# Performance work log

Measured on AMD Instinct MI355X. Metric: run time of the kernel, lower is better.

## Reference

```python
import jax, jax.numpy as jnp
import numpy as np

N = 100000
E = 1600000
IN_F = 128
HIDDEN = 128
HEADS = 2
N_CLASSES = 40
NEG_SLOPE = 0.2
BN_EPS = 1e-5


def setup_inputs() -> dict:
    key = jax.random.key(0)
    ks = jax.random.split(key, 12)
    c1 = HIDDEN // HEADS  # 64
    c2 = N_CLASSES        # 40 per head, concat=False
    inp = {
        "x": jax.random.normal(ks[0], (N, IN_F), dtype=jnp.float32),
        "edge_index": jax.random.randint(ks[1], (2, E), 0, N, dtype=jnp.int32),
        # layer 1 GATConv params
        "W1": jax.random.normal(ks[2], (IN_F, HEADS * c1), dtype=jnp.float32) * 0.05,
        "att_src1": jax.random.normal(ks[3], (HEADS, c1), dtype=jnp.float32) * 0.05,
        "att_dst1": jax.random.normal(ks[4], (HEADS, c1), dtype=jnp.float32) * 0.05,
        "b1": jnp.zeros((HEADS * c1,), dtype=jnp.float32),
        # BatchNorm params
        "gamma": jnp.ones((HIDDEN,), dtype=jnp.float32),
        "beta": jnp.zeros((HIDDEN,), dtype=jnp.float32),
        # layer 2 GATConv params (concat=False)
        "W2": jax.random.normal(ks[5], (HIDDEN, HEADS * c2), dtype=jnp.float32) * 0.05,
        "att_src2": jax.random.normal(ks[6], (HEADS, c2), dtype=jnp.float32) * 0.05,
        "att_dst2": jax.random.normal(ks[7], (HEADS, c2), dtype=jnp.float32) * 0.05,
        "b2": jnp.zeros((c2,), dtype=jnp.float32),
    }
    return inp


def gat_conv(x, src, dst, W, att_src, att_dst, bias, heads, concat):
    n = x.shape[0]
    h = (x @ W).reshape(n, heads, -1)             # [N, H, C]
    a_src = jnp.sum(h * att_src[None], axis=-1)   # [N, H]
    a_dst = jnp.sum(h * att_dst[None], axis=-1)   # [N, H]
    alpha = jax.nn.leaky_relu(a_src[src] + a_dst[dst], NEG_SLOPE)  # [E, H]
    # numerically-stable segment softmax over edges grouped by dst
    amax = jax.ops.segment_max(alpha, dst, num_segments=n)
    e = jnp.exp(alpha - amax[dst])
    denom = jax.ops.segment_sum(e, dst, num_segments=n)
    w = e / denom[dst]                            # [E, H]
    msg = h[src] * w[:, :, None]                  # [E, H, C]
    out = jax.ops.segment_sum(msg, dst, num_segments=n)  # [N, H, C]
    if concat:
        out = out.reshape(n, -1)
    else:
        out = out.mean(axis=1)
    return out + bias


def batch_norm(x, gamma, beta):
    mean = x.mean(axis=0)
    var = x.var(axis=0)
    return (x - mean) * jax.lax.rsqrt(var + BN_EPS) * gamma + beta


def reference(x, edge_index, W1, att_src1, att_dst1, b1, gamma, beta,
              W2, att_src2, att_dst2, b2):
    n = x.shape[0]
    # PyG GATConv default: add self-loops
    loops = jnp.arange(n, dtype=edge_index.dtype)
    src = jnp.concatenate([edge_index[0], loops])
    dst = jnp.concatenate([edge_index[1], loops])
    h = gat_conv(x, src, dst, W1, att_src1, att_dst1, b1, HEADS, concat=True)
    h = batch_norm(h, gamma, beta)
    h = gat_conv(h, src, dst, W2, att_src2, att_dst2, b2, HEADS, concat=False)
    return jax.nn.log_softmax(h, axis=1)
```

## Files before the change

kernel.cpp:

```cpp
#include <hip/hip_runtime.h>
#include <hip/hip_bf16.h>
#include <hip/hip_fp16.h>
#include <stdint.h>

#define N_NODES 100000
#define N_EDGES 1600000
#define ET (N_EDGES + N_NODES)
#define HID 128
#define C2 40
#define F2 80
#define NEG 0.2f
#define BN_EPS 1e-5f
#define NBUCK 391
#define BCAP 6144
#define NBB 640
#define EPB ((ET + NBB - 1) / NBB)
#define CHK 512

typedef __hip_bfloat16 bf16;
typedef __attribute__((ext_vector_type(8))) short s8v;
typedef __attribute__((ext_vector_type(4))) float f4v;
typedef __attribute__((ext_vector_type(4))) unsigned int u4v;
typedef __attribute__((ext_vector_type(2))) unsigned int u2v;

__device__ __forceinline__ float b2f(bf16 v){ return __bfloat162float(v); }
__device__ __forceinline__ float rdf(const void* p, size_t i, int isb){
    return isb ? b2f(((const bf16*)p)[i]) : ((const float*)p)[i];
}
__device__ __forceinline__ unsigned short f2bb(float v){
    bf16 h = __float2bfloat16(v);
    return *(unsigned short*)&h;
}
__device__ __forceinline__ uint32_t pack2(float a, float b){
    return (uint32_t)f2bb(a) | ((uint32_t)f2bb(b) << 16);
}
__device__ __forceinline__ uint32_t packh2(float a, float b){
    return (uint32_t)__half_as_ushort(__float2half(a))
         | ((uint32_t)__half_as_ushort(__float2half(b)) << 16);
}
__device__ __forceinline__ float lo16(uint32_t u){ return __uint_as_float(u << 16); }
__device__ __forceinline__ float hi16(uint32_t u){ return __uint_as_float(u & 0xFFFF0000u); }
__device__ __forceinline__ float hcvt(uint32_t w, int sh){
    return __half2float(__ushort_as_half((unsigned short)((w >> sh) & 0xFFFFu)));
}

__global__ __launch_bounds__(256) void k_init(
    const uint32_t* __restrict__ w1bits, int* __restrict__ flag,
    int* __restrict__ gcur, float* __restrict__ stats)
{
    __shared__ int cnt;
    int t = threadIdx.x;
    if (t == 0) cnt = 0;
    __syncthreads();
    uint32_t b = w1bits[t];
    float lo = __uint_as_float((b & 0xFFFFu) << 16);
    float a = fabsf(lo);
    if (a > 1e-8f && a < 1.0f) atomicAdd(&cnt, 1);
    for (int i = t; i < NBUCK; i += 256) gcur[i] = 0;
    stats[t] = 0.f;
    __syncthreads();
    if (t == 0) *flag = (cnt >= 192) ? 1 : 0;
}

__global__ __launch_bounds__(256) void k_gemm1(
    const void* __restrict__ x, const void* __restrict__ W1,
    const void* __restrict__ attS, const void* __restrict__ attD,
    const int* __restrict__ flag, unsigned short* __restrict__ h1,
    float* __restrict__ aS, float* __restrict__ aD)
{
    __shared__ __attribute__((aligned(16))) unsigned short wT[128*132];
    const int isb = *flag;
    const int tid = threadIdx.x;
    if (isb) {
        const unsigned short* w = (const unsigned short*)W1;
        for (int idx = tid; idx < 128*128; idx += 256){
            int k = idx >> 7, n = idx & 127;
            wT[n*132 + k] = w[idx];
        }
    } else {
        const float* w = (const float*)W1;
        for (int idx = tid; idx < 128*128; idx += 256){
            int k = idx >> 7, n = idx & 127;
            wT[n*132 + k] = f2bb(w[idx]);
        }
    }
    __syncthreads();

    const int w4 = tid >> 6, lane = tid & 63, quad = lane >> 4, l16 = lane & 15;
    const int rowbase = blockIdx.x*32 + (w4 >> 1)*16;
    const int colbase = (w4 & 1)*64;
    const int head = w4 & 1;

    s8v bfr[4][4];
    float asv[4], adv[4];
    #pragma unroll
    for (int ct = 0; ct < 4; ct++){
        int n = colbase + ct*16 + l16;
        asv[ct] = rdf(attS, n, isb);
        adv[ct] = rdf(attD, n, isb);
        #pragma unroll
        for (int s = 0; s < 4; s++){
            int k0 = s*32 + quad*8;
            const unsigned short* p = &wT[n*132 + k0];
            u2v a = *(const u2v*)p, b = *(const u2v*)(p+4);
            union { u4v u; s8v s; } cv; cv.u = (u4v){a[0],a[1],b[0],b[1]};
            bfr[ct][s] = cv.s;
        }
    }

    f4v acc[4];
    #pragma unroll
    for (int ct = 0; ct < 4; ct++) acc[ct] = (f4v){0.f,0.f,0.f,0.f};

    const int m = rowbase + l16;
    #pragma unroll
    for (int s = 0; s < 4; s++){
        int k0 = s*32 + quad*8;
        s8v af;
        if (isb){
            union { u4v u; s8v s; } cv;
            cv.u = *(const u4v*)((const unsigned short*)x + (size_t)m*128 + k0);
            af = cv.s;
        } else {
            const float* xp = (const float*)x + (size_t)m*128 + k0;
            f4v f0 = *(const f4v*)xp, f1 = *(const f4v*)(xp+4);
            union { u4v u; s8v s; } cv;
            cv.u = (u4v){pack2(f0[0],f0[1]), pack2(f0[2],f0[3]),
                         pack2(f1[0],f1[1]), pack2(f1[2],f1[3])};
            af = cv.s;
        }
        #pragma unroll
        for (int ct = 0; ct < 4; ct++)
            acc[ct] = __builtin_amdgcn_mfma_f32_16x16x32_bf16(af, bfr[ct][s], acc[ct], 0,0,0);
    }

    #pragma unroll
    for (int ct = 0; ct < 4; ct++){
        int col = colbase + ct*16 + l16;
        #pragma unroll
        for (int r = 0; r < 4; r++){
            int row = rowbase + quad*4 + r;
            h1[(size_t)row*128 + col] = f2bb(acc[ct][r]);
        }
    }

    #pragma unroll
    for (int r = 0; r < 4; r++){
        float vs = 0.f, vd = 0.f;
        #pragma unroll
        for (int ct = 0; ct < 4; ct++){ vs += acc[ct][r]*asv[ct]; vd += acc[ct][r]*adv[ct]; }
        #pragma unroll
        for (int o = 1; o < 16; o <<= 1){
            vs += __shfl_xor(vs, o, 64);
            vd += __shfl_xor(vd, o, 64);
        }
        if (l16 == 0){
            int row = rowbase + quad*4 + r;
            aS[row*2 + head] = vs;
            aD[row*2 + head] = vd;
        }
    }
}

__global__ __launch_bounds__(256) void k_bin(
    const int* __restrict__ esrc, const int* __restrict__ edst,
    int* __restrict__ gcur, uint32_t* __restrict__ staging)
{
    __shared__ int cnt[NBUCK];
    __shared__ int bb[NBUCK];
    const int t = threadIdx.x;
    for (int i = t; i < NBUCK; i += 256) cnt[i] = 0;
    __syncthreads();
    const int e0 = blockIdx.x * EPB;
    const int e1 = (e0 + EPB < ET) ? e0 + EPB : ET;
    for (int e = e0 + t; e < e1; e += 256){
        int d = (e < N_EDGES) ? edst[e] : e - N_EDGES;
        atomicAdd(&cnt[d >> 8], 1);
    }
    __syncthreads();
    const int bofs = (int)(blockIdx.x % NBUCK);
    for (int i = t; i < NBUCK; i += 256){
        int bkt = i + bofs; if (bkt >= NBUCK) bkt -= NBUCK;
        int c = cnt[bkt];
        bb[bkt] = c ? atomicAdd(&gcur[bkt], c) : 0;
        cnt[bkt] = 0;
    }
    __syncthreads();
    for (int e = e0 + t; e < e1; e += 256){
        int d, s;
        if (e < N_EDGES){ s = esrc[e]; d = edst[e]; } else { s = d = e - N_EDGES; }
        int b = d >> 8;
        int r = atomicAdd(&cnt[b], 1);
        int p = bb[b] + r;
        if (p < BCAP) staging[(size_t)b*BCAP + p] = ((uint32_t)s << 8) | (uint32_t)(d & 255);
    }
}

__global__ __launch_bounds__(256) void k_sort(
    const int* __restrict__ gcur, const uint32_t* __restrict__ staging,
    int* __restrict__ deg, int* __restrict__ cur, int* __restrict__ eidx)
{
    __shared__ int h[256], sc[256], rk[256];
    __shared__ int lsrc[BCAP];
    const int b = blockIdx.x;
    const int t = threadIdx.x;
    const int base = b * BCAP;
    int cnt = gcur[b];
    if (cnt > BCAP) cnt = BCAP;
    h[t] = 0; rk[t] = 0;
    __syncthreads();
    for (int i = t; i < cnt; i += 256)
        atomicAdd(&h[staging[base + i] & 255u], 1);
    __syncthreads();
    sc[t] = h[t];
    __syncthreads();
    for (int off = 1; off < 256; off <<= 1){
        int v = (t >= off) ? sc[t - off] : 0;
        __syncthreads();
        sc[t] += v;
        __syncthreads();
    }
    int dg = b*256 + t;
    if (dg < N_NODES){
        deg[dg] = h[t];
        cur[dg] = base + sc[t];
    }
    __syncthreads();
    for (int i = t; i < cnt; i += 256){
        uint32_t w = staging[base + i];
        int dl = w & 255u;
        int r = atomicAdd(&rk[dl], 1);
        lsrc[sc[dl] - h[dl] + r] = (int)(w >> 8);
    }
    __syncthreads();
    for (int i = t; i < cnt; i += 256) eidx[base + i] = lsrc[i];
}

__global__ __launch_bounds__(256) void k_agg1(
    const int* __restrict__ cur, const int* __restrict__ deg,
    const int* __restrict__ eidx, const float* __restrict__ aS,
    const float* __restrict__ aD, const uint32_t* __restrict__ h1u,
    uint32_t* __restrict__ out1u)
{
    __shared__ uint2 lse[4][CHK];
    const int wv = threadIdx.x >> 6;
    int d = blockIdx.x*4 + wv;
    if (d >= N_NODES) return;
    const int l = threadIdx.x & 63;
    int end   = __builtin_amdgcn_readfirstlane(cur[d]);
    int start = end - __builtin_amdgcn_readfirstlane(deg[d]);
    float2 ad = *(const float2*)(aD + d*2);
    const int sh = (l >= 32) ? 16 : 0;
    float den0 = 0.f, den1 = 0.f, acc0 = 0.f, acc1 = 0.f;

#define P1(P) { float Wf = hcvt((P).y, sh); uint32_t G = h1u[(size_t)(P).x*64 + l]; \
    acc0 += Wf * lo16(G); acc1 += Wf * hi16(G); }

    for (int c0 = start; c0 < end; c0 += CHK){
        int c1 = (c0 + CHK < end) ? c0 + CHK : end;
        int n = c1 - c0;
        for (int j = c0 + l; j < c1; j += 64){
            int s = eidx[j];
            float2 as = *(const float2*)(aS + s*2);
            float al0 = as.x + ad.x, al1 = as.y + ad.y;
            al0 = al0 > 0.f ? al0 : NEG*al0;
            al1 = al1 > 0.f ? al1 : NEG*al1;
            float e0 = __expf(al0), e1 = __expf(al1);
            lse[wv][j - c0] = make_uint2((uint32_t)s, packh2(e0, e1));
            den0 += e0; den1 += e1;
        }
        int i = 0;
        for (; i + 4 <= n; i += 4){
            uint2 p0 = lse[wv][i],   p1 = lse[wv][i+1];
            uint2 p2 = lse[wv][i+2], p3 = lse[wv][i+3];
            P1(p0); P1(p1); P1(p2); P1(p3);
        }
        for (; i < n; i++){ uint2 p = lse[wv][i]; P1(p); }
    }
#undef P1
    #pragma unroll
    for (int o = 1; o < 64; o <<= 1){
        den0 += __shfl_xor(den0, o, 64);
        den1 += __shfl_xor(den1, o, 64);
    }
    float r = 1.f / fmaxf((l < 32) ? den0 : den1, 1e-20f);
    out1u[(size_t)d*64 + l] = pack2(acc0*r, acc1*r);
}

__global__ __launch_bounds__(256) void k_bnstats(
    const uint32_t* __restrict__ out1u, float* __restrict__ stats)
{
    __shared__ float red[4][64][4];
    int fp = threadIdx.x & 63;
    int wv = threadIdx.x >> 6;
    float s0 = 0.f, q0 = 0.f, s1 = 0.f, q1 = 0.f;
    for (int r = blockIdx.x*4 + wv; r < N_NODES; r += 512){
        uint32_t u = out1u[(size_t)r*64 + fp];
        float f0 = lo16(u), f1 = hi16(u);
        s0 += f0; q0 += f0*f0; s1 += f1; q1 += f1*f1;
    }
    red[wv][fp][0] = s0; red[wv][fp][1] = s1;
    red[wv][fp][2] = q0; red[wv][fp][3] = q1;
    __syncthreads();
    if (threadIdx.x < 64){
        int l = threadIdx.x;
        float a0=0.f, a1=0.f, b0=0.f, b1=0.f;
        #pragma unroll
        for (int w = 0; w < 4; w++){
            a0 += red[w][l][0]; a1 += red[w][l][1];
            b0 += red[w][l][2]; b1 += red[w][l][3];
        }
        unsafeAtomicAdd(&stats[2*l],       a0);
        unsafeAtomicAdd(&stats[2*l+1],     a1);
        unsafeAtomicAdd(&stats[128+2*l],   b0);
        unsafeAtomicAdd(&stats[128+2*l+1], b1);
    }
}

__global__ __launch_bounds__(256) void k_gemm2(
    const unsigned short* __restrict__ out1b, const float* __restrict__ stats,
    const void* __restrict__ gamma, const void* __restrict__ beta,
    const void* __restrict__ W2, const void* __restrict__ attS,
    const void* __restrict__ attD, const int* __restrict__ flag,
    unsigned short* __restrict__ h2, float* __restrict__ aS, float* __restrict__ aD)
{
    __shared__ __attribute__((aligned(16))) unsigned short wT[80*132];
    __shared__ float scl[128], shl[128];
    const int isb = *flag;
    const int tid = threadIdx.x;
    for (int idx = tid; idx < 128*80; idx += 256){
        int k = idx / 80, n = idx - k*80;
        wT[n*132 + k] = isb ? ((const unsigned short*)W2)[idx]
                            : f2bb(((const float*)W2)[idx]);
    }
    if (tid < 128){
        float mean = stats[tid] * (1.f / N_NODES);
        float var = fmaxf(stats[128+tid] * (1.f / N_NODES) - mean*mean, 0.f);
        float rs = rsqrtf(var + BN_EPS);
        float sc = rdf(gamma, tid, isb) * rs;
        scl[tid] = sc;
        shl[tid] = rdf(beta, tid, isb) - mean*sc;
    }
    __syncthreads();

    const int w4 = tid >> 6, lane = tid & 63, quad = lane >> 4, l16 = lane & 15;
    const int rowbase = blockIdx.x*64 + w4*16;

    s8v bfr[5][4];
    float asv[5], adv[5];
    #pragma unroll
    for (int ct = 0; ct < 5; ct++){
        int n = ct*16 + l16;
        asv[ct] = rdf(attS, n, isb);
        adv[ct] = rdf(attD, n, isb);
        #pragma unroll
        for (int s = 0; s < 4; s++){
            int k0 = s*32 + quad*8;
            const unsigned short* p = &wT[n*132 + k0];
            u2v a = *(const u2v*)p, b = *(const u2v*)(p+4);
            union { u4v u; s8v s; } cv; cv.u = (u4v){a[0],a[1],b[0],b[1]};
            bfr[ct][s] = cv.s;
        }
    }

    f4v acc[5];
    #pragma unroll
    for (int ct = 0; ct < 5; ct++) acc[ct] = (f4v){0.f,0.f,0.f,0.f};

    int m = rowbase + l16;
    int mc = m < N_NODES ? m : N_NODES - 1;
    #pragma unroll
    for (int s = 0; s < 4; s++){
        int k0 = s*32 + quad*8;
        union { u4v u; s8v s8; } cin;
        cin.u = *(const u4v*)(out1b + (size_t)mc*128 + k0);
        u4v up;
        #pragma unroll
        for (int i = 0; i < 4; i++){
            float f0 = lo16(cin.u[i]), f1 = hi16(cin.u[i]);
            int k = k0 + 2*i;
            up[i] = pack2(f0*scl[k] + shl[k], f1*scl[k+1] + shl[k+1]);
        }
        union { u4v u; s8v s8; } cv; cv.u = up;
        #pragma unroll
        for (int ct = 0; ct < 5; ct++)
            acc[ct] = __builtin_amdgcn_mfma_f32_16x16x32_bf16(cv.s8, bfr[ct][s], acc[ct], 0,0,0);
    }

    #pragma unroll
    for (int ct = 0; ct < 5; ct++){
        int col = ct*16 + l16;
        #pragma unroll
        for (int r = 0; r < 4; r++){
            int row = rowbase + quad*4 + r;
            if (row < N_NODES) h2[(size_t)row*80 + col] = f2bb(acc[ct][r]);
        }
    }

    #pragma unroll
    for (int r = 0; r < 4; r++){
        float vs0 = 0.f, vs1 = 0.f, vd0 = 0.f, vd1 = 0.f;
        #pragma unroll
        for (int ct = 0; ct < 5; ct++){
            int col = ct*16 + l16;
            float ps = acc[ct][r]*asv[ct], pd = acc[ct][r]*adv[ct];
            if (col < 40){ vs0 += ps; vd0 += pd; } else { vs1 += ps; vd1 += pd; }
        }
        #pragma unroll
        for (int o = 1; o < 16; o <<= 1){
            vs0 += __shfl_xor(vs0, o, 64); vs1 += __shfl_xor(vs1, o, 64);
            vd0 += __shfl_xor(vd0, o, 64); vd1 += __shfl_xor(vd1, o, 64);
        }
        if (l16 == 0){
            int row = rowbase + quad*4 + r;
            if (row < N_NODES){
                aS[row*2 + 0] = vs0; aS[row*2 + 1] = vs1;
                aD[row*2 + 0] = vd0; aD[row*2 + 1] = vd1;
            }
        }
    }
}

__global__ __launch_bounds__(256) void k_agg2(
    const int* __restrict__ cur, const int* __restrict__ deg,
    const int* __restrict__ eidx, const float* __restrict__ aS,
    const float* __restrict__ aD, const uint32_t* __restrict__ h2u,
    const void* __restrict__ b2v, const int* __restrict__ flag,
    void* __restrict__ out)
{
    __shared__ uint2 lse[4][CHK];
    const int wv = threadIdx.x >> 6;
    int d = blockIdx.x*4 + wv;
    if (d >= N_NODES) return;
    const int l = threadIdx.x & 63;
    const int isb = *flag;
    int end   = __builtin_amdgcn_readfirstlane(cur[d]);
    int start = end - __builtin_amdgcn_readfirstlane(deg[d]);
    float2 ad = *(const float2*)(aD + d*2);
    const int sh = (l >= 20) ? 16 : 0;
    const bool act = l < 40;
    float den0 = 0.f, den1 = 0.f, acc0 = 0.f, acc1 = 0.f;

#define P2(P) { float Wf = hcvt((P).y, sh); \
    uint32_t G = act ? h2u[(size_t)(P).x*40 + l] : 0u; \
    acc0 += Wf * lo16(G); acc1 += Wf * hi16(G); }

    for (int c0 = start; c0 < end; c0 += CHK){
        int c1 = (c0 + CHK < end) ? c0 + CHK : end;
        int n = c1 - c0;
        for (int j = c0 + l; j < c1; j += 64){
            int s = eidx[j];
            float2 as = *(const float2*)(aS + s*2);
            float al0 = as.x + ad.x, al1 = as.y + ad.y;
            al0 = al0 > 0.f ? al0 : NEG*al0;
            al1 = al1 > 0.f ? al1 : NEG*al1;
            float e0 = __expf(al0), e1 = __expf(al1);
            lse[wv][j - c0] = make_uint2((uint32_t)s, packh2(e0, e1));
            den0 += e0; den1 += e1;
        }
        int i = 0;
        for (; i + 4 <= n; i += 4){
            uint2 p0 = lse[wv][i],   p1 = lse[wv][i+1];
            uint2 p2 = lse[wv][i+2], p3 = lse[wv][i+3];
            P2(p0); P2(p1); P2(p2); P2(p3);
        }
        for (; i < n; i++){ uint2 p = lse[wv][i]; P2(p); }
    }
#undef P2
    #pragma unroll
    for (int o = 1; o < 64; o <<= 1){
        den0 += __shfl_xor(den0, o, 64);
        den1 += __shfl_xor(den1, o, 64);
    }
    float r = 1.f / fmaxf((l < 20) ? den0 : den1, 1e-20f);
    acc0 *= r; acc1 *= r;

    float m0 = 0.5f*(acc0 + __shfl(acc0, l + 20, 64));
    float m1 = 0.5f*(acc1 + __shfl(acc1, l + 20, 64));
    float v0 = -1e30f, v1 = -1e30f;
    if (l < 20){
        v0 = m0 + rdf(b2v, 2*l,   isb);
        v1 = m1 + rdf(b2v, 2*l+1, isb);
    }
    float mx = fmaxf(v0, v1);
    #pragma unroll
    for (int o = 1; o < 32; o <<= 1) mx = fmaxf(mx, __shfl_xor(mx, o, 64));
    float ex = (l < 20) ? __expf(v0 - mx) + __expf(v1 - mx) : 0.f;
    #pragma unroll
    for (int o = 1; o < 32; o <<= 1) ex += __shfl_xor(ex, o, 64);
    float lse2 = __logf(ex);
    if (l < 20){
        float r0 = v0 - mx - lse2, r1 = v1 - mx - lse2;
        if (isb){
            ((uint32_t*)out)[(size_t)d*20 + l] = pack2(r0, r1);
        } else {
            float2 wr; wr.x = r0; wr.y = r1;
            ((float2*)out)[(size_t)d*20 + l] = wr;
        }
    }
}

extern "C" void kernel_launch(void* const* d_in, const int* in_sizes, int n_in,
                              void* d_out, int out_size, void* d_ws, size_t ws_size,
                              hipStream_t stream)
{
    const void* x    = d_in[0];
    const int*  ei   = (const int*)d_in[1];
    const void* W1   = d_in[2];
    const void* as1  = d_in[3];
    const void* ad1  = d_in[4];
    const void* gamma = d_in[6];
    const void* beta  = d_in[7];
    const void* W2   = d_in[8];
    const void* as2  = d_in[9];
    const void* ad2  = d_in[10];
    const void* b2v  = d_in[11];
    const int* esrc = ei;
    const int* edst = ei + N_EDGES;

    char* ws = (char*)d_ws;
    size_t off = 0;
    auto alloc = [&](size_t bytes) {
        void* p = ws + off;
        off += (bytes + 255) & ~(size_t)255;
        return p;
    };
    int*   flag  = (int*)alloc(256);
    float* stats = (float*)alloc(sizeof(float)*256);
    int*   gcur  = (int*)alloc(sizeof(int)*NBUCK);
    float* aS1   = (float*)alloc(sizeof(float)*N_NODES*2);
    float* aD1   = (float*)alloc(sizeof(float)*N_NODES*2);
    float* aS2   = (float*)alloc(sizeof(float)*N_NODES*2);
    float* aD2   = (float*)alloc(sizeof(float)*N_NODES*2);
    int*   deg   = (int*)alloc(sizeof(int)*N_NODES);
    int*   cur   = (int*)alloc(sizeof(int)*N_NODES);
    uint32_t* staging = (uint32_t*)alloc(sizeof(uint32_t)*(size_t)NBUCK*BCAP);
    int*   eidx  = (int*)alloc(sizeof(int)*(size_t)NBUCK*BCAP);
    unsigned short* h1  = (unsigned short*)alloc(2*(size_t)N_NODES*HID);
    unsigned short* out1 = (unsigned short*)alloc(2*(size_t)N_NODES*HID);
    unsigned short* h2  = h1;

    k_init<<<1, 256, 0, stream>>>((const uint32_t*)W1, flag, gcur, stats);
    k_gemm1<<<3125, 256, 0, stream>>>(x, W1, as1, ad1, flag, h1, aS1, aD1);
    k_bin<<<NBB, 256, 0, stream>>>(esrc, edst, gcur, staging);
    k_sort<<<NBUCK, 256, 0, stream>>>(gcur, staging, deg, cur, eidx);
    k_agg1<<<25000, 256, 0, stream>>>(cur, deg, eidx, aS1, aD1,
                                      (const uint32_t*)h1, (uint32_t*)out1);
    k_bnstats<<<128, 256, 0, stream>>>((const uint32_t*)out1, stats);
    k_gemm2<<<1563, 256, 0, stream>>>(out1, stats, gamma, beta, W2, as2, ad2,
                                      flag, h2, aS2, aD2);
    k_agg2<<<25000, 256, 0, stream>>>(cur, deg, eidx, aS2, aD2,
                                      (const uint32_t*)h2, b2v, flag, d_out);
}
```

Before: 435.1 us.

## Process multiple edges per wavefront with 16-byte gathers in aggregation kernels

Reworks both edge aggregation kernels so each wavefront splits into lane groups that handle different edges at once. Each lane gathers 16 bytes (8 bf16 features) per source row instead of 4 bytes, and partial sums are combined across groups with shuffles at the end. The aim is wider loads and more gathers in flight per wave, to hide latency on low-degree nodes. The cost is more registers, zero-padded LDS entries, extra cross-lane reductions, and in layer 2 four idle lanes because 64 lanes do not divide evenly into the 10-lane groups.

After: 423.9 us. -2.6%, faster.

```diff
diff --git a/kernel.cpp b/kernel.cpp
--- a/kernel.cpp
+++ b/kernel.cpp
@@ -242,19 +242,22 @@
     const float* __restrict__ aD, const uint32_t* __restrict__ h1u,
     uint32_t* __restrict__ out1u)
 {
-    __shared__ uint2 lse[4][CHK];
+    __shared__ uint2 lse[4][CHK + 8];
     const int wv = threadIdx.x >> 6;
     int d = blockIdx.x*4 + wv;
     if (d >= N_NODES) return;
     const int l = threadIdx.x & 63;
+    const int c = l & 15;
+    const int g = l >> 4;
     int end   = __builtin_amdgcn_readfirstlane(cur[d]);
     int start = end - __builtin_amdgcn_readfirstlane(deg[d]);
     float2 ad = *(const float2*)(aD + d*2);
-    const int sh = (l >= 32) ? 16 : 0;
-    float den0 = 0.f, den1 = 0.f, acc0 = 0.f, acc1 = 0.f;
-
-#define P1(P) { float Wf = hcvt((P).y, sh); uint32_t G = h1u[(size_t)(P).x*64 + l]; \
-    acc0 += Wf * lo16(G); acc1 += Wf * hi16(G); }
+    const int sh = (c >= 8) ? 16 : 0;
+    float den0 = 0.f, den1 = 0.f;
+    float acc[8];
+    #pragma unroll
+    for (int k = 0; k < 8; k++) acc[k] = 0.f;
+    const uint32_t* hc = h1u + 4*c;
 
     for (int c0 = start; c0 < end; c0 += CHK){
         int c1 = (c0 + CHK < end) ? c0 + CHK : end;
@@ -269,22 +272,54 @@
             lse[wv][j - c0] = make_uint2((uint32_t)s, packh2(e0, e1));
             den0 += e0; den1 += e1;
         }
+        int nn = (n + 3) & ~3;
+        if (l < nn - n) lse[wv][n + l] = make_uint2(0u, 0u);
         int i = 0;
-        for (; i + 4 <= n; i += 4){
-            uint2 p0 = lse[wv][i],   p1 = lse[wv][i+1];
-            uint2 p2 = lse[wv][i+2], p3 = lse[wv][i+3];
-            P1(p0); P1(p1); P1(p2); P1(p3);
-        }
-        for (; i < n; i++){ uint2 p = lse[wv][i]; P1(p); }
-    }
-#undef P1
+        for (; i + 4 < nn; i += 8){
+            uint2 pa = lse[wv][i + g];
+            uint2 pb = lse[wv][i + 4 + g];
+            u4v Ga = *(const u4v*)(hc + (size_t)pa.x*64);
+            u4v Gb = *(const u4v*)(hc + (size_t)pb.x*64);
+            float wa = hcvt(pa.y, sh), wb = hcvt(pb.y, sh);
+            #pragma unroll
+            for (int q = 0; q < 4; q++){
+                acc[2*q]   += wa * lo16(Ga[q]);
+                acc[2*q+1] += wa * hi16(Ga[q]);
+            }
+            #pragma unroll
+            for (int q = 0; q < 4; q++){
+                acc[2*q]   += wb * lo16(Gb[q]);
+                acc[2*q+1] += wb * hi16(Gb[q]);
+            }
+        }
+        if (i < nn){
+            uint2 pa = lse[wv][i + g];
+            u4v Ga = *(const u4v*)(hc + (size_t)pa.x*64);
+            float wa = hcvt(pa.y, sh);
+            #pragma unroll
+            for (int q = 0; q < 4; q++){
+                acc[2*q]   += wa * lo16(Ga[q]);
+                acc[2*q+1] += wa * hi16(Ga[q]);
+            }
+        }
+    }
     #pragma unroll
     for (int o = 1; o < 64; o <<= 1){
         den0 += __shfl_xor(den0, o, 64);
         den1 += __shfl_xor(den1, o, 64);
     }
-    float r = 1.f / fmaxf((l < 32) ? den0 : den1, 1e-20f);
-    out1u[(size_t)d*64 + l] = pack2(acc0*r, acc1*r);
+    #pragma unroll
+    for (int k = 0; k < 8; k++){
+        acc[k] += __shfl_xor(acc[k], 32, 64);
+        acc[k] += __shfl_xor(acc[k], 16, 64);
+    }
+    float r = 1.f / fmaxf((c < 8) ? den0 : den1, 1e-20f);
+    if (l < 16){
+        u4v o;
+        #pragma unroll
+        for (int q = 0; q < 4; q++) o[q] = pack2(acc[2*q]*r, acc[2*q+1]*r);
+        *(u4v*)(out1u + (size_t)d*64 + 4*c) = o;
+    }
 }
 
 __global__ __launch_bounds__(256) void k_bnstats(
@@ -428,22 +463,25 @@
     const void* __restrict__ b2v, const int* __restrict__ flag,
     void* __restrict__ out)
 {
-    __shared__ uint2 lse[4][CHK];
+    __shared__ uint2 lse[4][CHK + 8];
     const int wv = threadIdx.x >> 6;
     int d = blockIdx.x*4 + wv;
     if (d >= N_NODES) return;
     const int l = threadIdx.x & 63;
     const int isb = *flag;
+    const int c = l % 10;
+    const int g = l / 10;
+    const bool act = l < 60;
+    const int gq = act ? g : 0;
     int end   = __builtin_amdgcn_readfirstlane(cur[d]);
     int start = end - __builtin_amdgcn_readfirstlane(deg[d]);
     float2 ad = *(const float2*)(aD + d*2);
-    const int sh = (l >= 20) ? 16 : 0;
-    const bool act = l < 40;
-    float den0 = 0.f, den1 = 0.f, acc0 = 0.f, acc1 = 0.f;
-
-#define P2(P) { float Wf = hcvt((P).y, sh); \
-    uint32_t G = act ? h2u[(size_t)(P).x*40 + l] : 0u; \
-    acc0 += Wf * lo16(G); acc1 += Wf * hi16(G); }
+    const int sh = (c >= 5) ? 16 : 0;
+    float den0 = 0.f, den1 = 0.f;
+    float acc[8];
+    #pragma unroll
+    for (int k = 0; k < 8; k++) acc[k] = 0.f;
+    const uint32_t* hc = h2u + 4*c;
 
     for (int c0 = start; c0 < end; c0 += CHK){
         int c1 = (c0 + CHK < end) ? c0 + CHK : end;
@@ -458,44 +496,97 @@
             lse[wv][j - c0] = make_uint2((uint32_t)s, packh2(e0, e1));
             den0 += e0; den1 += e1;
         }
+        int nn = ((n + 5) / 6) * 6;
+        if (l < nn - n) lse[wv][n + l] = make_uint2(0u, 0u);
         int i = 0;
-        for (; i + 4 <= n; i += 4){
-            uint2 p0 = lse[wv][i],   p1 = lse[wv][i+1];
-            uint2 p2 = lse[wv][i+2], p3 = lse[wv][i+3];
-            P2(p0); P2(p1); P2(p2); P2(p3);
-        }
-        for (; i < n; i++){ uint2 p = lse[wv][i]; P2(p); }
-    }
-#undef P2
+        for (; i + 6 < nn; i += 12){
+            uint2 pa = lse[wv][i + gq];
+            uint2 pb = lse[wv][i + 6 + gq];
+            u4v Ga = *(const u4v*)(hc + (size_t)pa.x*40);
+            u4v Gb = *(const u4v*)(hc + (size_t)pb.x*40);
+            float wa = act ? hcvt(pa.y, sh) : 0.f;
+            float wb = act ? hcvt(pb.y, sh) : 0.f;
+            #pragma unroll
+            for (int q = 0; q < 4; q++){
+                acc[2*q]   += wa * lo16(Ga[q]);
+                acc[2*q+1] += wa * hi16(Ga[q]);
+            }
+            #pragma unroll
+            for (int q = 0; q < 4; q++){
+                acc[2*q]   += wb * lo16(Gb[q]);
+                acc[2*q+1] += wb * hi16(Gb[q]);
+            }
+        }
+        if (i < nn){
+            uint2 pa = lse[wv][i + gq];
+            u4v Ga = *(const u4v*)(hc + (size_t)pa.x*40);
+            float wa = act ? hcvt(pa.y, sh) : 0.f;
+            #pragma unroll
+            for (int q = 0; q < 4; q++){
+                acc[2*q]   += wa * lo16(Ga[q]);
+                acc[2*q+1] += wa * hi16(Ga[q]);
+            }
+        }
+    }
     #pragma unroll
     for (int o = 1; o < 64; o <<= 1){
         den0 += __shfl_xor(den0, o, 64);
         den1 += __shfl_xor(den1, o, 64);
     }
-    float r = 1.f / fmaxf((l < 20) ? den0 : den1, 1e-20f);
-    acc0 *= r; acc1 *= r;
-
-    float m0 = 0.5f*(acc0 + __shfl(acc0, l + 20, 64));
-    float m1 = 0.5f*(acc1 + __shfl(acc1, l + 20, 64));
-    float v0 = -1e30f, v1 = -1e30f;
-    if (l < 20){
-        v0 = m0 + rdf(b2v, 2*l,   isb);
-        v1 = m1 + rdf(b2v, 2*l+1, isb);
-    }
-    float mx = fmaxf(v0, v1);
-    #pragma unroll
-    for (int o = 1; o < 32; o <<= 1) mx = fmaxf(mx, __shfl_xor(mx, o, 64));
-    float ex = (l < 20) ? __expf(v0 - mx) + __expf(v1 - mx) : 0.f;
-    #pragma unroll
-    for (int o = 1; o < 32; o <<= 1) ex += __shfl_xor(ex, o, 64);
-    float lse2 = __logf(ex);
-    if (l < 20){
-        float r0 = v0 - mx - lse2, r1 = v1 - mx - lse2;
+    #pragma unroll
+    for (int k = 0; k < 8; k++){
+        float t = __shfl(acc[k], l + 30, 64);
+        acc[k] += (l < 30) ? t : 0.f;
+    }
+    #pragma unroll
+    for (int k = 0; k < 8; k++){
+        float t = __shfl(acc[k], l + 20, 64);
+        acc[k] += (l < 10) ? t : 0.f;
+    }
+    #pragma unroll
+    for (int k = 0; k < 8; k++){
+        float t = __shfl(acc[k], l + 10, 64);
+        acc[k] += (l < 10) ? t : 0.f;
+    }
+    float r = 1.f / fmaxf((c < 5) ? den0 : den1, 1e-20f);
+    #pragma unroll
+    for (int k = 0; k < 8; k++) acc[k] *= r;
+
+    int lb = (l < 5) ? l : 0;
+    float v[8];
+    float mx = -1e30f;
+    #pragma unroll
+    for (int k = 0; k < 8; k++){
+        float t = __shfl(acc[k], l + 5, 64);
+        v[k] = 0.5f*(acc[k] + t) + rdf(b2v, 8*lb + k, isb);
+        mx = fmaxf(mx, v[k]);
+    }
+    if (l >= 5) mx = -1e30f;
+    mx = fmaxf(mx, __shfl_xor(mx, 1, 64));
+    mx = fmaxf(mx, __shfl_xor(mx, 2, 64));
+    mx = fmaxf(mx, __shfl_xor(mx, 4, 64));
+    float ex = 0.f;
+    if (l < 5){
+        #pragma unroll
+        for (int k = 0; k < 8; k++) ex += __expf(v[k] - mx);
+    }
+    ex += __shfl_xor(ex, 1, 64);
+    ex += __shfl_xor(ex, 2, 64);
+    ex += __shfl_xor(ex, 4, 64);
+    float lsf = __logf(ex);
+    if (l < 5){
         if (isb){
-            ((uint32_t*)out)[(size_t)d*20 + l] = pack2(r0, r1);
+            u4v o;
+            #pragma unroll
+            for (int q = 0; q < 4; q++)
+                o[q] = pack2(v[2*q] - mx - lsf, v[2*q+1] - mx - lsf);
+            *(u4v*)((uint32_t*)out + (size_t)d*20 + 4*l) = o;
         } else {
-            float2 wr; wr.x = r0; wr.y = r1;
-            ((float2*)out)[(size_t)d*20 + l] = wr;
+            float4 o0, o1;
+            o0.x = v[0]-mx-lsf; o0.y = v[1]-mx-lsf; o0.z = v[2]-mx-lsf; o0.w = v[3]-mx-lsf;
+            o1.x = v[4]-mx-lsf; o1.y = v[5]-mx-lsf; o1.z = v[6]-mx-lsf; o1.w = v[7]-mx-lsf;
+            ((float4*)out)[(size_t)d*10 + 2*l]     = o0;
+            ((float4*)out)[(size_t)d*10 + 2*l + 1] = o1;
         }
     }
 }
```
